# Performance work log

Measured on AMD Instinct MI355X. Metric: run time of the kernel, lower is better.

## Reference

```python
import jax, jax.numpy as jnp
import numpy as np
import math

D_MODEL = 1024
NUM_HEADS = 16
D_K = D_MODEL // NUM_HEADS
B, S = 2, 2048


def setup_inputs() -> dict:
    key = jax.random.key(0)
    ks = jax.random.split(key, 13)
    scale = 1.0 / math.sqrt(D_MODEL)
    inp = {
        "q": jax.random.normal(ks[0], (B, S, D_MODEL), jnp.float32),
        "k": jax.random.normal(ks[1], (B, S, D_MODEL), jnp.float32),
        "v": jax.random.normal(ks[2], (B, S, D_MODEL), jnp.float32),
        "mask": jax.random.randint(ks[3], (B, 1, S, S), 0, 2, jnp.int32),
        # torch nn.Linear params: y = x @ W.T + b
        "wQ_w": jax.random.normal(ks[4], (D_MODEL, D_MODEL), jnp.float32) * scale,
        "wQ_b": jax.random.normal(ks[5], (D_MODEL,), jnp.float32) * scale,
        "wK_w": jax.random.normal(ks[6], (D_MODEL, D_MODEL), jnp.float32) * scale,
        "wK_b": jax.random.normal(ks[7], (D_MODEL,), jnp.float32) * scale,
        "wV_w": jax.random.normal(ks[8], (D_MODEL, D_MODEL), jnp.float32) * scale,
        "wV_b": jax.random.normal(ks[9], (D_MODEL,), jnp.float32) * scale,
        "wO_w": jax.random.normal(ks[10], (D_MODEL, D_MODEL), jnp.float32) * scale,
        "wO_b": jax.random.normal(ks[11], (D_MODEL,), jnp.float32) * scale,
    }
    return inp


def _split_heads(x):
    # [B, S, D] -> [B, H, S, dK]
    b, s, _ = x.shape
    return x.reshape(b, s, NUM_HEADS, D_K).transpose(0, 2, 1, 3)


def reference(q, k, v, mask, wQ_w, wQ_b, wK_w, wK_b, wV_w, wV_b, wO_w, wO_b):
    qh = _split_heads(q @ wQ_w.T + wQ_b)
    kh = _split_heads(k @ wK_w.T + wK_b)
    vh = _split_heads(v @ wV_w.T + wV_b)
    # scores: [B, H, S, S] -- materialized as in the original module
    scores = jnp.einsum("bhsd,bhtd->bhst", qh, kh) / math.sqrt(D_K)
    scores = jnp.where(mask == 0, jnp.float32(-1e9), scores)
    attn = jax.nn.softmax(scores, axis=-1)
    out = jnp.einsum("bhst,bhtd->bhsd", attn, vh)  # [B, H, S, dK]
    out = out.transpose(0, 2, 1, 3).reshape(q.shape[0], -1, D_MODEL)
    return out @ wO_w.T + wO_b
```

## Files before the change

### kernel.cpp

```cpp
#include <hip/hip_runtime.h>
#include <hip/hip_bf16.h>
#include <stdint.h>
#include <math.h>

#define NHEADS 16
#define DK 64
#define BATCH 2
#define SEQ 2048
#define DMODEL 1024
#define MROWS (BATCH*SEQ)

typedef __bf16 bf16x8 __attribute__((ext_vector_type(8)));
typedef float  f32x4  __attribute__((ext_vector_type(4)));
typedef float  f32x16 __attribute__((ext_vector_type(16)));

typedef const __attribute__((address_space(1))) void* gas_ptr;
typedef       __attribute__((address_space(3))) void* las_ptr;

__device__ __forceinline__ void async16(const void* g, void* l) {
  __builtin_amdgcn_global_load_lds((gas_ptr)g, (las_ptr)l, 16, 0, 0);
}

__device__ __forceinline__ unsigned short f2bf_raw(float f) {
  __hip_bfloat16 h = __float2bfloat16(f);
  return *reinterpret_cast<unsigned short*>(&h);
}

__device__ __forceinline__ uint32_t pk_bf16(float lo, float hi2) {
  uint32_t r;
  asm("v_cvt_pk_bf16_f32 %0, %1, %2" : "=v"(r) : "v"(lo), "v"(hi2));
  return r;
}

__device__ __forceinline__ void half_swap(uint32_t& a, uint32_t& b) {
  auto r = __builtin_amdgcn_permlane32_swap(a, b, false, false);
  a = (uint32_t)r[0];
  b = (uint32_t)r[1];
}

__device__ __forceinline__ float mask_sel(uint32_t msel, float s, float c) {
  uint32_t su = __float_as_uint(s), cu = __float_as_uint(c);
  return __uint_as_float((msel & su) | (~msel & cu));
}

__device__ __forceinline__ f32x16 zero16() {
  f32x16 z;
#pragma unroll
  for (int i = 0; i < 16; ++i) z[i] = 0.f;
  return z;
}

__global__ void cast_all_kernel(const float* __restrict__ q,
                                const float* __restrict__ k,
                                const float* __restrict__ v,
                                const float* __restrict__ w0,
                                const float* __restrict__ w1,
                                const float* __restrict__ w2,
                                const float* __restrict__ w3,
                                ushort4* __restrict__ out) {
  int i = blockIdx.x * 256 + threadIdx.x;
  const float* src;
  int local;
  if (i < 3145728) {
    int seg = i >> 20;
    src = (seg == 0) ? q : (seg == 1) ? k : v;
    local = i & 1048575;
  } else {
    int j = i - 3145728;
    int seg = j >> 18;
    src = (seg == 0) ? w0 : (seg == 1) ? w1 : (seg == 2) ? w2 : w3;
    local = j & 262143;
  }
  float4 f = reinterpret_cast<const float4*>(src)[local];
  ushort4 u;
  u.x = f2bf_raw(f.x); u.y = f2bf_raw(f.y);
  u.z = f2bf_raw(f.z); u.w = f2bf_raw(f.w);
  out[i] = u;
}

__global__ void pack_mask_kernel(const int* __restrict__ mask,
                                 uint32_t* __restrict__ bits) {
  int i = blockIdx.x * 256 + threadIdx.x;
  unsigned long long bal = __ballot(mask[i] != 0);
  int lane = threadIdx.x & 63;
  if (lane == 0)  bits[i >> 5] = (uint32_t)bal;
  if (lane == 32) bits[i >> 5] = (uint32_t)(bal >> 32);
}


__device__ __forceinline__ void gemm_core_128(
    const __hip_bfloat16* __restrict__ A, const __hip_bfloat16* __restrict__ Bw,
    int K, int m0, int n0,
    __hip_bfloat16* sA, __hip_bfloat16* sB, f32x4 acc[4][4]) {
  const int lane = threadIdx.x & 63;
  const int wid  = threadIdx.x >> 6;
  const int wr = wid >> 1, wc = wid & 1;
  const int crow = lane >> 2;
  const int ccol = (lane & 3) * 8;

#pragma unroll
  for (int mi = 0; mi < 4; ++mi)
#pragma unroll
    for (int ni = 0; ni < 4; ++ni) acc[mi][ni] = f32x4{0.f, 0.f, 0.f, 0.f};

  for (int k0 = 0; k0 < K; k0 += 32) {
    for (int c = wid; c < 8; c += 4) {
      async16(A  + (size_t)(m0 + c * 16 + crow) * K + k0 + ccol,
              (char*)sA + c * 1024 + lane * 16);
      async16(Bw + (size_t)(n0 + c * 16 + crow) * K + k0 + ccol,
              (char*)sB + c * 1024 + lane * 16);
    }
    __syncthreads();
    bf16x8 af[4], bfr[4];
#pragma unroll
    for (int mi = 0; mi < 4; ++mi)
      af[mi] = *reinterpret_cast<const bf16x8*>(
          &sA[(wr * 64 + mi * 16 + (lane & 15)) * 32 + 8 * (lane >> 4)]);
#pragma unroll
    for (int ni = 0; ni < 4; ++ni)
      bfr[ni] = *reinterpret_cast<const bf16x8*>(
          &sB[(wc * 64 + ni * 16 + (lane & 15)) * 32 + 8 * (lane >> 4)]);
    __builtin_amdgcn_s_setprio(1);
#pragma unroll
    for (int mi = 0; mi < 4; ++mi)
#pragma unroll
      for (int ni = 0; ni < 4; ++ni)
        acc[mi][ni] = __builtin_amdgcn_mfma_f32_16x16x32_bf16(
            af[mi], bfr[ni], acc[mi][ni], 0, 0, 0);
    __builtin_amdgcn_s_setprio(0);
    __syncthreads();
  }
}

__global__ __launch_bounds__(256, 3) void qkv_gemm_kernel(
    const __hip_bfloat16* __restrict__ Xq, const __hip_bfloat16* __restrict__ Xk,
    const __hip_bfloat16* __restrict__ Xv,
    const __hip_bfloat16* __restrict__ Wq, const __hip_bfloat16* __restrict__ Wk,
    const __hip_bfloat16* __restrict__ Wv,
    const float* __restrict__ bq, const float* __restrict__ bk,
    const float* __restrict__ bv,
    __hip_bfloat16* __restrict__ Qh, __hip_bfloat16* __restrict__ Kh,
    __hip_bfloat16* __restrict__ VhT) {
  __shared__ __hip_bfloat16 sA[128 * 32];
  __shared__ __hip_bfloat16 sB[128 * 32];
  const int z = blockIdx.z;
  const __hip_bfloat16* A  = (z == 0) ? Xq : (z == 1) ? Xk : Xv;
  const __hip_bfloat16* Bw = (z == 0) ? Wq : (z == 1) ? Wk : Wv;
  const float* bias        = (z == 0) ? bq : (z == 1) ? bk : bv;
  __hip_bfloat16* Co       = (z == 0) ? Qh : (z == 1) ? Kh : VhT;
  const int m0 = blockIdx.x * 128, n0 = blockIdx.y * 128;
  f32x4 acc[4][4];
  gemm_core_128(A, Bw, DMODEL, m0, n0, sA, sB, acc);

  const int lane = threadIdx.x & 63, wid = threadIdx.x >> 6;
  const int wr = wid >> 1, wc = wid & 1;
  const int l15 = lane & 15, lg = lane >> 4;
  const float osc = (z == 0) ? 0.18033688f : 1.0f;
  if (z != 2) {
#pragma unroll
    for (int mi = 0; mi < 4; ++mi)
#pragma unroll
      for (int ni = 0; ni < 4; ++ni) {
        int j = n0 + wc * 64 + ni * 16 + l15;
        float bj = bias[j];
        int hh = j >> 6, d = j & 63;
#pragma unroll
        for (int r = 0; r < 4; ++r) {
          int i = m0 + wr * 64 + mi * 16 + lg * 4 + r;
          int bb = i >> 11, s = i & 2047;
          float v = (acc[mi][ni][r] + bj) * osc;
          Co[((size_t)(bb * NHEADS + hh) * SEQ + s) * DK + d] = __float2bfloat16(v);
        }
      }
  } else {
#pragma unroll
    for (int mi = 0; mi < 4; ++mi)
#pragma unroll
      for (int ni = 0; ni < 4; ++ni) {
        int j = n0 + wc * 64 + ni * 16 + l15;
        float bj = bias[j];
        int hh = j >> 6, d = j & 63;
        int i0 = m0 + wr * 64 + mi * 16 + lg * 4;
        int bb = i0 >> 11, sbase = i0 & 2047;
        ushort4 st;
        st.x = f2bf_raw(acc[mi][ni][0] + bj);
        st.y = f2bf_raw(acc[mi][ni][1] + bj);
        st.z = f2bf_raw(acc[mi][ni][2] + bj);
        st.w = f2bf_raw(acc[mi][ni][3] + bj);
        *reinterpret_cast<ushort4*>(
            &Co[((size_t)(bb * NHEADS + hh) * DK + d) * SEQ + sbase]) = st;
      }
  }
}

__global__ __launch_bounds__(256, 3) void out_gemm_kernel(
    const __hip_bfloat16* __restrict__ A, const __hip_bfloat16* __restrict__ Ww,
    const float* __restrict__ bias, float* __restrict__ C) {
  __shared__ __hip_bfloat16 sA[128 * 32];
  __shared__ __hip_bfloat16 sB[128 * 32];
  const int m0 = blockIdx.x * 128, n0 = blockIdx.y * 128;
  f32x4 acc[4][4];
  gemm_core_128(A, Ww, DMODEL, m0, n0, sA, sB, acc);
  const int lane = threadIdx.x & 63, wid = threadIdx.x >> 6;
  const int wr = wid >> 1, wc = wid & 1;
#pragma unroll
  for (int mi = 0; mi < 4; ++mi)
#pragma unroll
    for (int ni = 0; ni < 4; ++ni) {
      int j = n0 + wc * 64 + ni * 16 + (lane & 15);
      float bj = bias[j];
#pragma unroll
      for (int r = 0; r < 4; ++r) {
        int i = m0 + wr * 64 + mi * 16 + (lane >> 4) * 4 + r;
        C[(size_t)i * DMODEL + j] = acc[mi][ni][r] + bj;
      }
    }
}


__global__ __launch_bounds__(256, 2) void attn_kernel(
    const __hip_bfloat16* __restrict__ Qh, const __hip_bfloat16* __restrict__ Kh,
    const __hip_bfloat16* __restrict__ VhT, const uint32_t* __restrict__ mbits,
    __hip_bfloat16* __restrict__ AO) {
  __shared__ __hip_bfloat16 Ks[2][64 * 64];
  __shared__ __hip_bfloat16 Vs[2][64 * 64];
  __shared__ float sRed[4 * 32];

  const int tid = threadIdx.x, lane = tid & 63, wid = tid >> 6;
  const int l31 = lane & 31, hi = lane >> 5;
  const int sw = l31 & 7;
  const int bh = blockIdx.y, b = bh >> 4, h = bh & 15;
  const int q0g = blockIdx.x * 128 + wid * 32;

  const __hip_bfloat16* Qp = Qh  + (size_t)bh * SEQ * DK;
  const __hip_bfloat16* Kp = Kh  + (size_t)bh * SEQ * DK;
  const __hip_bfloat16* Vp = VhT + (size_t)bh * DK * SEQ;
  const uint32_t* mb = mbits + (size_t)b * SEQ * (SEQ / 32)
                             + (size_t)(q0g + l31) * (SEQ / 32);
  float* sRedW = &sRed[wid * 32];

  bf16x8 qf[4];
#pragma unroll
  for (int dc = 0; dc < 4; ++dc)
    qf[dc] = *reinterpret_cast<const bf16x8*>(
        &Qp[(size_t)(q0g + l31) * DK + dc * 16 + hi * 8]);

  f32x16 acc0 = zero16(), acc1 = zero16();
  float l_run = 0.f;

#define STAGE(kv0_, s_)                                                        \
  {                                                                            \
    _Pragma("unroll")                                                          \
    for (int u = 0; u < 2; ++u) {                                              \
      int c = tid + u * 256;                                                   \
      int row = c >> 3, ss = (c & 7) ^ (row & 7);                              \
      async16(Kp + (size_t)(kv0_ + row) * DK + ss * 8,                         \
              (char*)Ks[s_] + c * 16);                                         \
      async16(Vp + (size_t)row * SEQ + (kv0_) + ss * 8,                        \
              (char*)Vs[s_] + c * 16);                                         \
    }                                                                          \
  }

  STAGE(0, 0);
  uint2 mw = *reinterpret_cast<const uint2*>(mb);
  asm volatile("s_waitcnt vmcnt(0)" ::: "memory");
  __syncthreads();

  const int NT = SEQ / 64;
  for (int t = 0; t < NT; ++t) {
    const int cur = t & 1;
    if (t + 1 < NT) STAGE((t + 1) * 64, cur ^ 1);

    uint2 mw_next;
    if (t + 1 < NT) mw_next = *reinterpret_cast<const uint2*>(mb + (t + 1) * 2);
    uint32_t w0 = mw.x >> (4 * hi), w1 = mw.y >> (4 * hi);

    const __hip_bfloat16* ks = Ks[cur];
    const __hip_bfloat16* vs = Vs[cur];

    f32x16 s0 = zero16(), s1 = zero16();
    __builtin_amdgcn_s_setprio(1);
#pragma unroll
    for (int dc = 0; dc < 4; ++dc) {
      bf16x8 k0 = *reinterpret_cast<const bf16x8*>(
          &ks[(size_t)(l31) * 64 + (((dc * 2 + hi) ^ sw) * 8)]);
      bf16x8 k1 = *reinterpret_cast<const bf16x8*>(
          &ks[(size_t)(32 + l31) * 64 + (((dc * 2 + hi) ^ sw) * 8)]);
      s0 = __builtin_amdgcn_mfma_f32_32x32x16_bf16(k0, qf[dc], s0, 0, 0, 0);
      s1 = __builtin_amdgcn_mfma_f32_32x32x16_bf16(k1, qf[dc], s1, 0, 0, 0);
    }
    __builtin_amdgcn_s_setprio(0);

    uint32_t pa0[4], pa1[4], pa2[4], pa3[4];
    {
      float p[16];
#pragma unroll
      for (int r = 0; r < 16; ++r) {
        const int sh = (r & 3) + 8 * (r >> 2);
        uint32_t msel = (uint32_t)__builtin_amdgcn_sbfe((int)w0, sh, 1);
        p[r] = exp2f(mask_sel(msel, s0[r], -1e9f));
        l_run += p[r];
      }
      uint32_t a0 = pk_bf16(p[0], p[1]),  a1 = pk_bf16(p[2], p[3]);
      uint32_t b0 = pk_bf16(p[4], p[5]),  b1 = pk_bf16(p[6], p[7]);
      uint32_t c0 = pk_bf16(p[8], p[9]),  c1 = pk_bf16(p[10], p[11]);
      uint32_t d0 = pk_bf16(p[12], p[13]), d1 = pk_bf16(p[14], p[15]);
      half_swap(a0, b0); half_swap(a1, b1);
      half_swap(c0, d0); half_swap(c1, d1);
      pa0[0] = a0; pa0[1] = a1; pa0[2] = b0; pa0[3] = b1;
      pa1[0] = c0; pa1[1] = c1; pa1[2] = d0; pa1[3] = d1;
    }
    {
      float p[16];
#pragma unroll
      for (int r = 0; r < 16; ++r) {
        const int sh = (r & 3) + 8 * (r >> 2);
        uint32_t msel = (uint32_t)__builtin_amdgcn_sbfe((int)w1, sh, 1);
        p[r] = exp2f(mask_sel(msel, s1[r], -1e9f));
        l_run += p[r];
      }
      uint32_t a0 = pk_bf16(p[0], p[1]),  a1 = pk_bf16(p[2], p[3]);
      uint32_t b0 = pk_bf16(p[4], p[5]),  b1 = pk_bf16(p[6], p[7]);
      uint32_t c0 = pk_bf16(p[8], p[9]),  c1 = pk_bf16(p[10], p[11]);
      uint32_t d0 = pk_bf16(p[12], p[13]), d1 = pk_bf16(p[14], p[15]);
      half_swap(a0, b0); half_swap(a1, b1);
      half_swap(c0, d0); half_swap(c1, d1);
      pa2[0] = a0; pa2[1] = a1; pa2[2] = b0; pa2[3] = b1;
      pa3[0] = c0; pa3[1] = c1; pa3[2] = d0; pa3[3] = d1;
    }

    union { uint32_t u[4]; bf16x8 v; } pc;
    __builtin_amdgcn_s_setprio(1);
#pragma unroll
    for (int tt = 0; tt < 4; ++tt) {
      const uint32_t* pw = (tt == 0) ? pa0 : (tt == 1) ? pa1 : (tt == 2) ? pa2 : pa3;
      pc.u[0] = pw[0]; pc.u[1] = pw[1]; pc.u[2] = pw[2]; pc.u[3] = pw[3];
      bf16x8 v0 = *reinterpret_cast<const bf16x8*>(
          &vs[(size_t)(l31) * 64 + (((2 * tt + hi) ^ sw) * 8)]);
      bf16x8 v1 = *reinterpret_cast<const bf16x8*>(
          &vs[(size_t)(32 + l31) * 64 + (((2 * tt + hi) ^ sw) * 8)]);
      acc0 = __builtin_amdgcn_mfma_f32_32x32x16_bf16(pc.v, v0, acc0, 0, 0, 0);
      acc1 = __builtin_amdgcn_mfma_f32_32x32x16_bf16(pc.v, v1, acc1, 0, 0, 0);
    }
    __builtin_amdgcn_s_setprio(0);

    mw = mw_next;
    asm volatile("s_waitcnt vmcnt(0)" ::: "memory");
    __syncthreads();
  }

  l_run += __shfl_xor(l_run, 32);
  if (hi == 0) sRedW[l31] = l_run;
  asm volatile("s_waitcnt lgkmcnt(0)" ::: "memory");
  __syncthreads();
#pragma unroll
  for (int r = 0; r < 16; ++r) {
    int cr = (r & 3) + 8 * (r >> 2) + 4 * hi;
    float linv = 1.0f / sRedW[cr];
    int qrow = q0g + cr;
    size_t base = ((size_t)b * SEQ + qrow) * DMODEL + h * 64 + l31;
    AO[base]      = __float2bfloat16(acc0[r] * linv);
    AO[base + 32] = __float2bfloat16(acc1[r] * linv);
  }
}


extern "C" void kernel_launch(void* const* d_in, const int* in_sizes, int n_in,
                              void* d_out, int out_size, void* d_ws, size_t ws_size,
                              hipStream_t stream) {
  const float* q    = (const float*)d_in[0];
  const float* k    = (const float*)d_in[1];
  const float* v    = (const float*)d_in[2];
  const int*   mask = (const int*)d_in[3];
  const float* wQ_w = (const float*)d_in[4];
  const float* wQ_b = (const float*)d_in[5];
  const float* wK_w = (const float*)d_in[6];
  const float* wK_b = (const float*)d_in[7];
  const float* wV_w = (const float*)d_in[8];
  const float* wV_b = (const float*)d_in[9];
  const float* wO_w = (const float*)d_in[10];
  const float* wO_b = (const float*)d_in[11];

  char* ws = (char*)d_ws;
  const size_t SZ_X = (size_t)MROWS * DMODEL * 2;
  const size_t SZ_W = (size_t)DMODEL * DMODEL * 2;
  __hip_bfloat16* Xq  = (__hip_bfloat16*)(ws);
  __hip_bfloat16* Xk  = (__hip_bfloat16*)(ws + SZ_X);
  __hip_bfloat16* Xv  = (__hip_bfloat16*)(ws + 2 * SZ_X);
  __hip_bfloat16* Wq  = (__hip_bfloat16*)(ws + 3 * SZ_X);
  __hip_bfloat16* Wk  = (__hip_bfloat16*)(ws + 3 * SZ_X + SZ_W);
  __hip_bfloat16* Wv  = (__hip_bfloat16*)(ws + 3 * SZ_X + 2 * SZ_W);
  __hip_bfloat16* Wo  = (__hip_bfloat16*)(ws + 3 * SZ_X + 3 * SZ_W);
  __hip_bfloat16* Qh  = (__hip_bfloat16*)(ws + 3 * SZ_X + 4 * SZ_W);
  __hip_bfloat16* Kh  = (__hip_bfloat16*)(ws + 4 * SZ_X + 4 * SZ_W);
  __hip_bfloat16* VhT = (__hip_bfloat16*)(ws + 5 * SZ_X + 4 * SZ_W);
  __hip_bfloat16* AO  = (__hip_bfloat16*)(ws + 6 * SZ_X + 4 * SZ_W);
  uint32_t*       MB  = (uint32_t*)      (ws + 7 * SZ_X + 4 * SZ_W);

  cast_all_kernel<<<16384, 256, 0, stream>>>(q, k, v, wQ_w, wK_w, wV_w, wO_w,
                                             (ushort4*)ws);
  pack_mask_kernel<<<(BATCH * SEQ * SEQ) / 256, 256, 0, stream>>>(mask, MB);

  qkv_gemm_kernel<<<dim3(MROWS / 128, DMODEL / 128, 3), 256, 0, stream>>>(
      Xq, Xk, Xv, Wq, Wk, Wv, wQ_b, wK_b, wV_b, Qh, Kh, VhT);

  attn_kernel<<<dim3(SEQ / 128, BATCH * NHEADS), 256, 0, stream>>>(
      Qh, Kh, VhT, MB, AO);

  out_gemm_kernel<<<dim3(MROWS / 128, DMODEL / 128), 256, 0, stream>>>(
      AO, Wo, wO_b, (float*)d_out);
}
```

Baseline: 290.8 us.

## Merge cast and mask-pack kernels, interleave PV MFMAs, use native exp2, raise occupancy

Folds the fp32-to-bf16 cast kernel and the mask bit-packing kernel into one prep launch, removing a kernel launch and the gap between them. In the attention loop, exp2f becomes the hardware v_exp_f32 builtin, and each half's P·V MFMAs are issued right after that half's probabilities are packed, so less packed P has to stay live. The launch bound for attention goes from 2 to 3 blocks per CU. Register pressure under the tighter bound could cause spills, and the native exp2 may lose a little accuracy for very negative inputs.

```diff
diff --git a/kernel.cpp b/kernel.cpp
--- a/kernel.cpp
+++ b/kernel.cpp
@@ -26,6 +26,16 @@
   return *reinterpret_cast<unsigned short*>(&h);
 }
 
+__device__ __forceinline__ float fast_exp2(float x) {
+#if __has_builtin(__builtin_amdgcn_exp2f)
+  return __builtin_amdgcn_exp2f(x);
+#else
+  float r;
+  asm("v_exp_f32 %0, %1\ns_nop 1" : "=v"(r) : "v"(x));
+  return r;
+#endif
+}
+
 __device__ __forceinline__ uint32_t pk_bf16(float lo, float hi2) {
   uint32_t r;
   asm("v_cvt_pk_bf16_f32 %0, %1, %2" : "=v"(r) : "v"(lo), "v"(hi2));
@@ -50,41 +60,42 @@
   return z;
 }
 
-__global__ void cast_all_kernel(const float* __restrict__ q,
-                                const float* __restrict__ k,
-                                const float* __restrict__ v,
-                                const float* __restrict__ w0,
-                                const float* __restrict__ w1,
-                                const float* __restrict__ w2,
-                                const float* __restrict__ w3,
-                                ushort4* __restrict__ out) {
-  int i = blockIdx.x * 256 + threadIdx.x;
-  const float* src;
-  int local;
-  if (i < 3145728) {
-    int seg = i >> 20;
-    src = (seg == 0) ? q : (seg == 1) ? k : v;
-    local = i & 1048575;
+__global__ void prep_kernel(const float* __restrict__ q,
+                            const float* __restrict__ k,
+                            const float* __restrict__ v,
+                            const float* __restrict__ w0,
+                            const float* __restrict__ w1,
+                            const float* __restrict__ w2,
+                            const float* __restrict__ w3,
+                            ushort4* __restrict__ out,
+                            const int* __restrict__ mask,
+                            uint32_t* __restrict__ bits) {
+  if (blockIdx.x < 16384) {
+    int i = blockIdx.x * 256 + threadIdx.x;
+    const float* src;
+    int local;
+    if (i < 3145728) {
+      int seg = i >> 20;
+      src = (seg == 0) ? q : (seg == 1) ? k : v;
+      local = i & 1048575;
+    } else {
+      int j = i - 3145728;
+      int seg = j >> 18;
+      src = (seg == 0) ? w0 : (seg == 1) ? w1 : (seg == 2) ? w2 : w3;
+      local = j & 262143;
+    }
+    float4 f = reinterpret_cast<const float4*>(src)[local];
+    ushort4 u;
+    u.x = f2bf_raw(f.x); u.y = f2bf_raw(f.y);
+    u.z = f2bf_raw(f.z); u.w = f2bf_raw(f.w);
+    out[i] = u;
   } else {
-    int j = i - 3145728;
-    int seg = j >> 18;
-    src = (seg == 0) ? w0 : (seg == 1) ? w1 : (seg == 2) ? w2 : w3;
-    local = j & 262143;
-  }
-  float4 f = reinterpret_cast<const float4*>(src)[local];
-  ushort4 u;
-  u.x = f2bf_raw(f.x); u.y = f2bf_raw(f.y);
-  u.z = f2bf_raw(f.z); u.w = f2bf_raw(f.w);
-  out[i] = u;
-}
-
-__global__ void pack_mask_kernel(const int* __restrict__ mask,
-                                 uint32_t* __restrict__ bits) {
-  int i = blockIdx.x * 256 + threadIdx.x;
-  unsigned long long bal = __ballot(mask[i] != 0);
-  int lane = threadIdx.x & 63;
-  if (lane == 0)  bits[i >> 5] = (uint32_t)bal;
-  if (lane == 32) bits[i >> 5] = (uint32_t)(bal >> 32);
+    int i = (blockIdx.x - 16384) * 256 + threadIdx.x;
+    unsigned long long bal = __ballot(mask[i] != 0);
+    int lane = threadIdx.x & 63;
+    if (lane == 0)  bits[i >> 5] = (uint32_t)bal;
+    if (lane == 32) bits[i >> 5] = (uint32_t)(bal >> 32);
+  }
 }
 
 
@@ -218,7 +229,7 @@
 }
 
 
-__global__ __launch_bounds__(256, 2) void attn_kernel(
+__global__ __launch_bounds__(256, 3) void attn_kernel(
     const __hip_bfloat16* __restrict__ Qh, const __hip_bfloat16* __restrict__ Kh,
     const __hip_bfloat16* __restrict__ VhT, const uint32_t* __restrict__ mbits,
     __hip_bfloat16* __restrict__ AO) {
@@ -291,14 +302,14 @@
     }
     __builtin_amdgcn_s_setprio(0);
 
-    uint32_t pa0[4], pa1[4], pa2[4], pa3[4];
+    union { uint32_t u[4]; bf16x8 v; } pc;
     {
       float p[16];
 #pragma unroll
       for (int r = 0; r < 16; ++r) {
         const int sh = (r & 3) + 8 * (r >> 2);
         uint32_t msel = (uint32_t)__builtin_amdgcn_sbfe((int)w0, sh, 1);
-        p[r] = exp2f(mask_sel(msel, s0[r], -1e9f));
+        p[r] = fast_exp2(mask_sel(msel, s0[r], -1e9f));
         l_run += p[r];
       }
       uint32_t a0 = pk_bf16(p[0], p[1]),  a1 = pk_bf16(p[2], p[3]);
@@ -307,8 +318,26 @@
       uint32_t d0 = pk_bf16(p[12], p[13]), d1 = pk_bf16(p[14], p[15]);
       half_swap(a0, b0); half_swap(a1, b1);
       half_swap(c0, d0); half_swap(c1, d1);
-      pa0[0] = a0; pa0[1] = a1; pa0[2] = b0; pa0[3] = b1;
-      pa1[0] = c0; pa1[1] = c1; pa1[2] = d0; pa1[3] = d1;
+      __builtin_amdgcn_s_setprio(1);
+      pc.u[0] = a0; pc.u[1] = a1; pc.u[2] = b0; pc.u[3] = b1;
+      {
+        bf16x8 v0 = *reinterpret_cast<const bf16x8*>(
+            &vs[(size_t)(l31) * 64 + (((0 + hi) ^ sw) * 8)]);
+        bf16x8 v1 = *reinterpret_cast<const bf16x8*>(
+            &vs[(size_t)(32 + l31) * 64 + (((0 + hi) ^ sw) * 8)]);
+        acc0 = __builtin_amdgcn_mfma_f32_32x32x16_bf16(pc.v, v0, acc0, 0, 0, 0);
+        acc1 = __builtin_amdgcn_mfma_f32_32x32x16_bf16(pc.v, v1, acc1, 0, 0, 0);
+      }
+      pc.u[0] = c0; pc.u[1] = c1; pc.u[2] = d0; pc.u[3] = d1;
+      {
+        bf16x8 v0 = *reinterpret_cast<const bf16x8*>(
+            &vs[(size_t)(l31) * 64 + (((2 + hi) ^ sw) * 8)]);
+        bf16x8 v1 = *reinterpret_cast<const bf16x8*>(
+            &vs[(size_t)(32 + l31) * 64 + (((2 + hi) ^ sw) * 8)]);
+        acc0 = __builtin_amdgcn_mfma_f32_32x32x16_bf16(pc.v, v0, acc0, 0, 0, 0);
+        acc1 = __builtin_amdgcn_mfma_f32_32x32x16_bf16(pc.v, v1, acc1, 0, 0, 0);
+      }
+      __builtin_amdgcn_s_setprio(0);
     }
     {
       float p[16];
@@ -316,7 +345,7 @@
       for (int r = 0; r < 16; ++r) {
         const int sh = (r & 3) + 8 * (r >> 2);
         uint32_t msel = (uint32_t)__builtin_amdgcn_sbfe((int)w1, sh, 1);
-        p[r] = exp2f(mask_sel(msel, s1[r], -1e9f));
+        p[r] = fast_exp2(mask_sel(msel, s1[r], -1e9f));
         l_run += p[r];
       }
       uint32_t a0 = pk_bf16(p[0], p[1]),  a1 = pk_bf16(p[2], p[3]);
@@ -325,24 +354,27 @@
       uint32_t d0 = pk_bf16(p[12], p[13]), d1 = pk_bf16(p[14], p[15]);
       half_swap(a0, b0); half_swap(a1, b1);
       half_swap(c0, d0); half_swap(c1, d1);
-      pa2[0] = a0; pa2[1] = a1; pa2[2] = b0; pa2[3] = b1;
-      pa3[0] = c0; pa3[1] = c1; pa3[2] = d0; pa3[3] = d1;
-    }
-
-    union { uint32_t u[4]; bf16x8 v; } pc;
-    __builtin_amdgcn_s_setprio(1);
-#pragma unroll
-    for (int tt = 0; tt < 4; ++tt) {
-      const uint32_t* pw = (tt == 0) ? pa0 : (tt == 1) ? pa1 : (tt == 2) ? pa2 : pa3;
-      pc.u[0] = pw[0]; pc.u[1] = pw[1]; pc.u[2] = pw[2]; pc.u[3] = pw[3];
-      bf16x8 v0 = *reinterpret_cast<const bf16x8*>(
-          &vs[(size_t)(l31) * 64 + (((2 * tt + hi) ^ sw) * 8)]);
-      bf16x8 v1 = *reinterpret_cast<const bf16x8*>(
-          &vs[(size_t)(32 + l31) * 64 + (((2 * tt + hi) ^ sw) * 8)]);
-      acc0 = __builtin_amdgcn_mfma_f32_32x32x16_bf16(pc.v, v0, acc0, 0, 0, 0);
-      acc1 = __builtin_amdgcn_mfma_f32_32x32x16_bf16(pc.v, v1, acc1, 0, 0, 0);
-    }
-    __builtin_amdgcn_s_setprio(0);
+      __builtin_amdgcn_s_setprio(1);
+      pc.u[0] = a0; pc.u[1] = a1; pc.u[2] = b0; pc.u[3] = b1;
+      {
+        bf16x8 v0 = *reinterpret_cast<const bf16x8*>(
+            &vs[(size_t)(l31) * 64 + (((4 + hi) ^ sw) * 8)]);
+        bf16x8 v1 = *reinterpret_cast<const bf16x8*>(
+            &vs[(size_t)(32 + l31) * 64 + (((4 + hi) ^ sw) * 8)]);
+        acc0 = __builtin_amdgcn_mfma_f32_32x32x16_bf16(pc.v, v0, acc0, 0, 0, 0);
+        acc1 = __builtin_amdgcn_mfma_f32_32x32x16_bf16(pc.v, v1, acc1, 0, 0, 0);
+      }
+      pc.u[0] = c0; pc.u[1] = c1; pc.u[2] = d0; pc.u[3] = d1;
+      {
+        bf16x8 v0 = *reinterpret_cast<const bf16x8*>(
+            &vs[(size_t)(l31) * 64 + (((6 + hi) ^ sw) * 8)]);
+        bf16x8 v1 = *reinterpret_cast<const bf16x8*>(
+            &vs[(size_t)(32 + l31) * 64 + (((6 + hi) ^ sw) * 8)]);
+        acc0 = __builtin_amdgcn_mfma_f32_32x32x16_bf16(pc.v, v0, acc0, 0, 0, 0);
+        acc1 = __builtin_amdgcn_mfma_f32_32x32x16_bf16(pc.v, v1, acc1, 0, 0, 0);
+      }
+      __builtin_amdgcn_s_setprio(0);
+    }
 
     mw = mw_next;
     asm volatile("s_waitcnt vmcnt(0)" ::: "memory");
@@ -397,9 +429,8 @@
   __hip_bfloat16* AO  = (__hip_bfloat16*)(ws + 6 * SZ_X + 4 * SZ_W);
   uint32_t*       MB  = (uint32_t*)      (ws + 7 * SZ_X + 4 * SZ_W);
 
-  cast_all_kernel<<<16384, 256, 0, stream>>>(q, k, v, wQ_w, wK_w, wV_w, wO_w,
-                                             (ushort4*)ws);
-  pack_mask_kernel<<<(BATCH * SEQ * SEQ) / 256, 256, 0, stream>>>(mask, MB);
+  prep_kernel<<<49152, 256, 0, stream>>>(q, k, v, wQ_w, wK_w, wV_w, wO_w,
+                                         (ushort4*)ws, mask, MB);
 
   qkv_gemm_kernel<<<dim3(MROWS / 128, DMODEL / 128, 3), 256, 0, stream>>>(
       Xq, Xk, Xv, Wq, Wk, Wv, wQ_b, wK_b, wV_b, Qh, Kh, VhT);
```

After: 267.3 us. -8.1%, faster.
